# Kernel tuning notes

Measured on AMD Instinct MI355X. Metric: run time of the kernel, lower is better.

## Reference

```python
import jax, jax.numpy as jnp
import numpy as np

P, B, N, M, D_LAT = 4, 32, 2048, 512, 128
BETA = 1e-3
BIG = 1e9  # sentinel for masked-out pairwise distances


def quat_to_rotmat(q):
    # q: (..., 4) quaternion (w, x, y, z), normalized then converted
    q = q / jnp.linalg.norm(q, axis=-1, keepdims=True)
    w, x, y, z = q[..., 0], q[..., 1], q[..., 2], q[..., 3]
    R = jnp.stack([
        1 - 2 * (y * y + z * z), 2 * (x * y - w * z), 2 * (x * z + w * y),
        2 * (x * y + w * z), 1 - 2 * (x * x + z * z), 2 * (y * z - w * x),
        2 * (x * z - w * y), 2 * (y * z + w * x), 1 - 2 * (x * x + y * y),
    ], axis=-1)
    return R.reshape(q.shape[:-1] + (3, 3))


def setup_inputs() -> dict:
    key = jax.random.key(0)
    ks = jax.random.split(key, 8)
    return {
        'ipt': jax.random.normal(ks[0], (B, N, 3), jnp.float32),
        'opt': jax.random.normal(ks[1], (P, B, M, 3), jnp.float32),
        'trans': jax.random.normal(ks[2], (P, B, 3), jnp.float32),
        'rots': jax.random.normal(ks[3], (P, B, 4), jnp.float32),
        'probs': jax.random.uniform(ks[4], (P, B, 1), jnp.float32),
        'idx': jax.random.randint(ks[5], (B, N), 0, P),
        'mu': jax.random.normal(ks[6], (B, D_LAT), jnp.float32),
        'logvar': jax.random.normal(ks[7], (B, D_LAT), jnp.float32),
    }


def _parts_distance(ipt, opt, trans, rots, probs, idx):
    # Masked, fully-batched equivalent of the original python double loop:
    # index_select by (idx==i) + _remove_zero_rows are expressed as boolean
    # masks; empty part/sample combinations are excluded via `valid`.
    chamfer_d = 0.0
    coverage = 0.0
    quality = 0.0
    num = 0.0
    nonzero_x = jnp.any(ipt != 0, axis=-1)  # (B, N)
    for i in range(P):  # fixed small part count, structurally distinct slices
        y = opt[i]                                   # (B, M, 3)
        mask_y = jnp.any(y != 0, axis=-1)            # (B, M) _remove_zero_rows
        mx = (idx == i) & nonzero_x                  # (B, N) part selection
        # transform_to_primitives_centric_system: x_local = R (x - t)
        R = quat_to_rotmat(rots[i])                  # (B, 3, 3)
        x = jnp.einsum('bij,bnj->bni', R, ipt - trans[i][:, None, :])
        # pairwise squared distances, (B, N, M)
        D = jnp.sum((x[:, :, None, :] - y[:, None, :, :]) ** 2, axis=-1)
        nx = jnp.sum(mx, axis=-1)                    # (B,)
        ny = jnp.sum(mask_y, axis=-1)                # (B,)
        # quality: mean over valid x of min distance to valid y
        qual = jnp.sum(jnp.where(mx, jnp.min(jnp.where(mask_y[:, None, :], D, BIG), axis=-1), 0.0), axis=-1) / jnp.maximum(nx, 1)
        # coverage: mean over valid y of min distance to valid x
        cov = jnp.sum(jnp.where(mask_y, jnp.min(jnp.where(mx[:, :, None], D, BIG), axis=-2), 0.0), axis=-1) / jnp.maximum(ny, 1)
        cd = qual + cov                              # symmetric chamfer
        valid = (nx > 0) & (ny > 0)                  # x.size(0)!=0 and y.size(0)!=0
        w = jnp.where(valid, probs[i][:, 0], 0.0)    # prob-weighted sum over batch
        n = jnp.sum(valid).astype(jnp.float32)
        has = (n > 0).astype(jnp.float32)
        inv_n = has / jnp.maximum(n, 1.0)
        chamfer_d = chamfer_d + jnp.sum(w * cd) * inv_n
        coverage = coverage + jnp.sum(w * cov) * inv_n
        quality = quality + jnp.sum(w * qual) * inv_n
        num = num + has
    inv_num = 1.0 / jnp.maximum(num, 1.0)
    return chamfer_d * inv_num, coverage * inv_num, quality * inv_num


def KL(mu, logvar):
    # standard VAE KL: sum over latent, mean over batch
    return -0.5 * jnp.sum(1.0 + logvar - mu ** 2 - jnp.exp(logvar)) / mu.shape[0]


def reference(ipt, opt, trans, rots, probs, idx, mu, logvar):
    cds, covs, quals = _parts_distance(ipt, opt, trans, rots, probs, idx)
    kld = KL(mu, logvar)
    return (cds + BETA * kld, cds, covs, quals, kld)
```

## Files before the change

kernel.cpp:

```cpp
#include <hip/hip_runtime.h>
#include <math.h>

#define PP 4
#define BB 32
#define NN 2048
#define MM 512
#define DLAT 128
#define BETA_C 1e-3f
#define BIGV 1e9f
#define THREADS 512

__device__ float g_ws[4 * PP * BB];

__device__ __forceinline__ float dist2f4(float4 a, float4 b) {
    float dx = a.x - b.x, dy = a.y - b.y, dz = a.z - b.z;
    return dx * dx + dy * dy + dz * dz;
}

__global__ __launch_bounds__(THREADS) void parts_kernel(
    const float* __restrict__ ipt,
    const float* __restrict__ opt,
    const float* __restrict__ trans,
    const float* __restrict__ rots,
    const int*   __restrict__ idx)
{
    const int b = blockIdx.x;
    const int i = blockIdx.y;
    const int phase = blockIdx.z;
    const int tid = threadIdx.x;

    __shared__ float Rm[9], tv[3];
    __shared__ int s_nx, s_ny;
    __shared__ float4 sy[MM];
    __shared__ float4 sx[NN];
    __shared__ float red[THREADS / 64];

    if (tid == 0) {
        s_nx = 0;
        s_ny = 0;
        const float* q = rots + (i * BB + b) * 4;
        float qw = q[0], qx = q[1], qy = q[2], qz = q[3];
        float inv = 1.0f / sqrtf(qw * qw + qx * qx + qy * qy + qz * qz);
        qw *= inv; qx *= inv; qy *= inv; qz *= inv;
        Rm[0] = 1.0f - 2.0f * (qy * qy + qz * qz);
        Rm[1] = 2.0f * (qx * qy - qw * qz);
        Rm[2] = 2.0f * (qx * qz + qw * qy);
        Rm[3] = 2.0f * (qx * qy + qw * qz);
        Rm[4] = 1.0f - 2.0f * (qx * qx + qz * qz);
        Rm[5] = 2.0f * (qy * qz - qw * qx);
        Rm[6] = 2.0f * (qx * qz - qw * qy);
        Rm[7] = 2.0f * (qy * qz + qw * qx);
        Rm[8] = 1.0f - 2.0f * (qx * qx + qy * qy);
        const float* t = trans + (i * BB + b) * 3;
        tv[0] = t[0]; tv[1] = t[1]; tv[2] = t[2];
    }
    __syncthreads();

    int cnt = 0;
    for (int m = tid; m < MM; m += THREADS) {
        const float* y = opt + (((size_t)i * BB + b) * MM + m) * 3;
        float yx = y[0], yy = y[1], yz = y[2];
        bool v = (yx != 0.0f) | (yy != 0.0f) | (yz != 0.0f);
        if (v) cnt++;
        else { yx = 1e8f; yy = 1e8f; yz = 1e8f; }
        sy[m] = make_float4(yx, yy, yz, v ? 1.0f : 0.0f);
    }
    if (cnt) atomicAdd(&s_ny, cnt);

    const float R0 = Rm[0], R1 = Rm[1], R2 = Rm[2];
    const float R3 = Rm[3], R4 = Rm[4], R5 = Rm[5];
    const float R6 = Rm[6], R7 = Rm[7], R8 = Rm[8];
    const float t0 = tv[0], t1 = tv[1], t2 = tv[2];
    for (int n = tid; n < NN; n += THREADS) {
        const float* p = ipt + ((size_t)b * NN + n) * 3;
        float px = p[0], py = p[1], pz = p[2];
        bool nz = (px != 0.0f) | (py != 0.0f) | (pz != 0.0f);
        if (nz && idx[b * NN + n] == i) {
            px -= t0; py -= t1; pz -= t2;
            float lx = R0 * px + R1 * py + R2 * pz;
            float ly = R3 * px + R4 * py + R5 * pz;
            float lz = R6 * px + R7 * py + R8 * pz;
            int pos = atomicAdd(&s_nx, 1);
            sx[pos] = make_float4(lx, ly, lz, 0.0f);
        }
    }
    __syncthreads();
    const int nx = s_nx;
    const int ny = s_ny;

    float sum = 0.0f;
    if (phase == 0) {
        for (int k = tid; k < nx; k += THREADS) {
            float4 p = sx[k];
            float m0 = BIGV, m1 = BIGV, m2 = BIGV, m3 = BIGV;
            for (int m = 0; m < MM; m += 4) {
                m0 = fminf(m0, dist2f4(p, sy[m]));
                m1 = fminf(m1, dist2f4(p, sy[m + 1]));
                m2 = fminf(m2, dist2f4(p, sy[m + 2]));
                m3 = fminf(m3, dist2f4(p, sy[m + 3]));
            }
            sum += fminf(fminf(m0, m1), fminf(m2, m3));
        }
    } else {
        for (int m = tid; m < MM; m += THREADS) {
            float4 q = sy[m];
            if (q.w != 0.0f) {
                float m0 = BIGV, m1 = BIGV, m2 = BIGV, m3 = BIGV;
                int k = 0;
                for (; k + 4 <= nx; k += 4) {
                    m0 = fminf(m0, dist2f4(q, sx[k]));
                    m1 = fminf(m1, dist2f4(q, sx[k + 1]));
                    m2 = fminf(m2, dist2f4(q, sx[k + 2]));
                    m3 = fminf(m3, dist2f4(q, sx[k + 3]));
                }
                float dmin = fminf(fminf(m0, m1), fminf(m2, m3));
                for (; k < nx; ++k) dmin = fminf(dmin, dist2f4(q, sx[k]));
                sum += dmin;
            }
        }
    }

    for (int off = 32; off > 0; off >>= 1) sum += __shfl_down(sum, off);
    if ((tid & 63) == 0) red[tid >> 6] = sum;
    __syncthreads();
    if (tid == 0) {
        float tot = 0.0f;
        for (int w = 0; w < THREADS / 64; ++w) tot += red[w];
        int pb = i * BB + b;
        if (phase == 0) {
            g_ws[pb] = tot;
            g_ws[2 * PP * BB + pb] = (float)nx;
        } else {
            g_ws[PP * BB + pb] = tot;
            g_ws[3 * PP * BB + pb] = (float)ny;
        }
    }
}

__global__ __launch_bounds__(256) void finalize_kernel(
    const float* __restrict__ probs,
    const float* __restrict__ mu,
    const float* __restrict__ logvar,
    float* __restrict__ out)
{
    const int tid = threadIdx.x;
    __shared__ float red[4];
    __shared__ float s_wq[PP * BB], s_wc[PP * BB], s_val[PP * BB];

    float kls = 0.0f;
    for (int t = tid; t < BB * DLAT; t += 256) {
        float m_ = mu[t], lv = logvar[t];
        kls += 1.0f + lv - m_ * m_ - expf(lv);
    }
    for (int off = 32; off > 0; off >>= 1) kls += __shfl_down(kls, off);
    if ((tid & 63) == 0) red[tid >> 6] = kls;

    if (tid < PP * BB) {
        float qs = g_ws[tid];
        float cs = g_ws[PP * BB + tid];
        float nxf = g_ws[2 * PP * BB + tid];
        float nyf = g_ws[3 * PP * BB + tid];
        bool valid = (nxf > 0.0f) && (nyf > 0.0f);
        float w = valid ? probs[tid] : 0.0f;
        s_wq[tid] = w * (qs / fmaxf(nxf, 1.0f));
        s_wc[tid] = w * (cs / fmaxf(nyf, 1.0f));
        s_val[tid] = valid ? 1.0f : 0.0f;
    }
    __syncthreads();

    if (tid == 0) {
        float kld = -0.5f * (red[0] + red[1] + red[2] + red[3]) / (float)BB;
        float ch = 0.0f, cov = 0.0f, qu = 0.0f, num = 0.0f;
        for (int i = 0; i < PP; ++i) {
            float sq = 0.0f, sc = 0.0f, n = 0.0f;
            for (int bb = 0; bb < BB; ++bb) {
                sq += s_wq[i * BB + bb];
                sc += s_wc[i * BB + bb];
                n += s_val[i * BB + bb];
            }
            float has = (n > 0.0f) ? 1.0f : 0.0f;
            float invn = has / fmaxf(n, 1.0f);
            qu += sq * invn;
            cov += sc * invn;
            ch += (sq + sc) * invn;
            num += has;
        }
        float invnum = 1.0f / fmaxf(num, 1.0f);
        float cds = ch * invnum;
        out[0] = cds + BETA_C * kld;
        out[1] = cds;
        out[2] = cov * invnum;
        out[3] = qu * invnum;
        out[4] = kld;
    }
}

extern "C" void kernel_launch(void* const* d_in, const int* in_sizes, int n_in,
                              void* d_out, int out_size, void* d_ws, size_t ws_size,
                              hipStream_t stream) {
    const float* ipt    = (const float*)d_in[0];
    const float* opt    = (const float*)d_in[1];
    const float* trans  = (const float*)d_in[2];
    const float* rots   = (const float*)d_in[3];
    const float* probs  = (const float*)d_in[4];
    const int*   idx    = (const int*)d_in[5];
    const float* mu     = (const float*)d_in[6];
    const float* logvar = (const float*)d_in[7];
    float* out = (float*)d_out;
    (void)d_ws; (void)ws_size; (void)in_sizes; (void)n_in; (void)out_size;

    dim3 grid(BB, PP, 2);
    parts_kernel<<<grid, THREADS, 0, stream>>>(ipt, opt, trans, rots, idx);
    finalize_kernel<<<1, 256, 0, stream>>>(probs, mu, logvar, out);
}
```

Measured before the change: 108.6 us.

## Register-tile pairwise distance loops with SoA shared layout and 256-thread blocks

Switches the shared point buffers from float4 AoS to separate x/y/z arrays so each step loads four candidate coordinates with vector reads. Each thread now keeps several query points in registers and reuses every loaded target quad across them, raising arithmetic per shared-memory load. Block size drops to 256 threads, and the target array is padded with sentinels to a multiple of four so the tail loop goes away. In exchange it uses more registers per thread and gives fewer threads per block for the bandwidth-light setup phase.

```diff
diff --git a/kernel.cpp b/kernel.cpp
--- a/kernel.cpp
+++ b/kernel.cpp
@@ -8,13 +8,89 @@
 #define DLAT 128
 #define BETA_C 1e-3f
 #define BIGV 1e9f
-#define THREADS 512
+#define SENT 1e8f
+#define THREADS 256
 
 __device__ float g_ws[4 * PP * BB];
 
-__device__ __forceinline__ float dist2f4(float4 a, float4 b) {
-    float dx = a.x - b.x, dy = a.y - b.y, dz = a.z - b.z;
-    return dx * dx + dy * dy + dz * dz;
+template<int SLOTS>
+__device__ __forceinline__ float quality_pass(
+    const float* __restrict__ syx, const float* __restrict__ syy, const float* __restrict__ syz,
+    const float* __restrict__ sxx, const float* __restrict__ sxy, const float* __restrict__ sxz,
+    int nx, int base, int tid)
+{
+    float px[SLOTS], py[SLOTS], pz[SLOTS], mna[SLOTS], mnb[SLOTS];
+    bool act[SLOTS];
+#pragma unroll
+    for (int s = 0; s < SLOTS; ++s) {
+        int k = base + s * THREADS + tid;
+        act[s] = (k < nx);
+        px[s] = act[s] ? sxx[k] : SENT;
+        py[s] = act[s] ? sxy[k] : SENT;
+        pz[s] = act[s] ? sxz[k] : SENT;
+        mna[s] = BIGV; mnb[s] = BIGV;
+    }
+    for (int m = 0; m < MM; m += 4) {
+        float4 yx = *reinterpret_cast<const float4*>(syx + m);
+        float4 yy = *reinterpret_cast<const float4*>(syy + m);
+        float4 yz = *reinterpret_cast<const float4*>(syz + m);
+#pragma unroll
+        for (int s = 0; s < SLOTS; ++s) {
+            float dx0 = px[s] - yx.x, dy0 = py[s] - yy.x, dz0 = pz[s] - yz.x;
+            float dx1 = px[s] - yx.y, dy1 = py[s] - yy.y, dz1 = pz[s] - yz.y;
+            float dx2 = px[s] - yx.z, dy2 = py[s] - yy.z, dz2 = pz[s] - yz.z;
+            float dx3 = px[s] - yx.w, dy3 = py[s] - yy.w, dz3 = pz[s] - yz.w;
+            float d0 = dx0 * dx0 + dy0 * dy0 + dz0 * dz0;
+            float d1 = dx1 * dx1 + dy1 * dy1 + dz1 * dz1;
+            float d2 = dx2 * dx2 + dy2 * dy2 + dz2 * dz2;
+            float d3 = dx3 * dx3 + dy3 * dy3 + dz3 * dz3;
+            mna[s] = fminf(mna[s], fminf(d0, d1));
+            mnb[s] = fminf(mnb[s], fminf(d2, d3));
+        }
+    }
+    float sum = 0.0f;
+#pragma unroll
+    for (int s = 0; s < SLOTS; ++s)
+        if (act[s]) sum += fminf(mna[s], mnb[s]);
+    return sum;
+}
+
+__device__ __forceinline__ float coverage_pass(
+    const float* __restrict__ syx, const float* __restrict__ syy, const float* __restrict__ syz,
+    const float* __restrict__ sxx, const float* __restrict__ sxy, const float* __restrict__ sxz,
+    int nx4, int tid)
+{
+    float qx[2], qy[2], qz[2], mna[2], mnb[2];
+#pragma unroll
+    for (int s = 0; s < 2; ++s) {
+        int m = s * THREADS + tid;
+        qx[s] = syx[m]; qy[s] = syy[m]; qz[s] = syz[m];
+        mna[s] = BIGV; mnb[s] = BIGV;
+    }
+    for (int k = 0; k < nx4; k += 4) {
+        float4 xx = *reinterpret_cast<const float4*>(sxx + k);
+        float4 xy = *reinterpret_cast<const float4*>(sxy + k);
+        float4 xz = *reinterpret_cast<const float4*>(sxz + k);
+#pragma unroll
+        for (int s = 0; s < 2; ++s) {
+            float dx0 = qx[s] - xx.x, dy0 = qy[s] - xy.x, dz0 = qz[s] - xz.x;
+            float dx1 = qx[s] - xx.y, dy1 = qy[s] - xy.y, dz1 = qz[s] - xz.y;
+            float dx2 = qx[s] - xx.z, dy2 = qy[s] - xy.z, dz2 = qz[s] - xz.z;
+            float dx3 = qx[s] - xx.w, dy3 = qy[s] - xy.w, dz3 = qz[s] - xz.w;
+            float d0 = dx0 * dx0 + dy0 * dy0 + dz0 * dz0;
+            float d1 = dx1 * dx1 + dy1 * dy1 + dz1 * dz1;
+            float d2 = dx2 * dx2 + dy2 * dy2 + dz2 * dz2;
+            float d3 = dx3 * dx3 + dy3 * dy3 + dz3 * dz3;
+            mna[s] = fminf(mna[s], fminf(d0, d1));
+            mnb[s] = fminf(mnb[s], fminf(d2, d3));
+        }
+    }
+    float sum = 0.0f;
+#pragma unroll
+    for (int s = 0; s < 2; ++s)
+        if (qx[s] != SENT)
+            sum += fminf(mna[s], mnb[s]);
+    return sum;
 }
 
 __global__ __launch_bounds__(THREADS) void parts_kernel(
@@ -29,10 +105,10 @@
     const int phase = blockIdx.z;
     const int tid = threadIdx.x;
 
-    __shared__ float Rm[9], tv[3];
+    __shared__ float Rm[12];
     __shared__ int s_nx, s_ny;
-    __shared__ float4 sy[MM];
-    __shared__ float4 sx[NN];
+    __shared__ __align__(16) float syx[MM], syy[MM], syz[MM];
+    __shared__ __align__(16) float sxx[NN], sxy[NN], sxz[NN];
     __shared__ float red[THREADS / 64];
 
     if (tid == 0) {
@@ -52,7 +128,7 @@
         Rm[7] = 2.0f * (qy * qz + qw * qx);
         Rm[8] = 1.0f - 2.0f * (qx * qx + qy * qy);
         const float* t = trans + (i * BB + b) * 3;
-        tv[0] = t[0]; tv[1] = t[1]; tv[2] = t[2];
+        Rm[9] = t[0]; Rm[10] = t[1]; Rm[11] = t[2];
     }
     __syncthreads();
 
@@ -62,62 +138,47 @@
         float yx = y[0], yy = y[1], yz = y[2];
         bool v = (yx != 0.0f) | (yy != 0.0f) | (yz != 0.0f);
         if (v) cnt++;
-        else { yx = 1e8f; yy = 1e8f; yz = 1e8f; }
-        sy[m] = make_float4(yx, yy, yz, v ? 1.0f : 0.0f);
+        else { yx = SENT; yy = SENT; yz = SENT; }
+        syx[m] = yx; syy[m] = yy; syz[m] = yz;
     }
     if (cnt) atomicAdd(&s_ny, cnt);
 
     const float R0 = Rm[0], R1 = Rm[1], R2 = Rm[2];
     const float R3 = Rm[3], R4 = Rm[4], R5 = Rm[5];
     const float R6 = Rm[6], R7 = Rm[7], R8 = Rm[8];
-    const float t0 = tv[0], t1 = tv[1], t2 = tv[2];
+    const float t0 = Rm[9], t1 = Rm[10], t2 = Rm[11];
     for (int n = tid; n < NN; n += THREADS) {
         const float* p = ipt + ((size_t)b * NN + n) * 3;
         float px = p[0], py = p[1], pz = p[2];
         bool nz = (px != 0.0f) | (py != 0.0f) | (pz != 0.0f);
         if (nz && idx[b * NN + n] == i) {
             px -= t0; py -= t1; pz -= t2;
-            float lx = R0 * px + R1 * py + R2 * pz;
-            float ly = R3 * px + R4 * py + R5 * pz;
-            float lz = R6 * px + R7 * py + R8 * pz;
             int pos = atomicAdd(&s_nx, 1);
-            sx[pos] = make_float4(lx, ly, lz, 0.0f);
+            sxx[pos] = R0 * px + R1 * py + R2 * pz;
+            sxy[pos] = R3 * px + R4 * py + R5 * pz;
+            sxz[pos] = R6 * px + R7 * py + R8 * pz;
         }
     }
     __syncthreads();
     const int nx = s_nx;
     const int ny = s_ny;
-
-    float sum = 0.0f;
+    const int nx4 = (nx + 3) & ~3;
+    if (tid < nx4 - nx) {
+        sxx[nx + tid] = SENT; sxy[nx + tid] = SENT; sxz[nx + tid] = SENT;
+    }
+    __syncthreads();
+
+    float sum;
     if (phase == 0) {
-        for (int k = tid; k < nx; k += THREADS) {
-            float4 p = sx[k];
-            float m0 = BIGV, m1 = BIGV, m2 = BIGV, m3 = BIGV;
-            for (int m = 0; m < MM; m += 4) {
-                m0 = fminf(m0, dist2f4(p, sy[m]));
-                m1 = fminf(m1, dist2f4(p, sy[m + 1]));
-                m2 = fminf(m2, dist2f4(p, sy[m + 2]));
-                m3 = fminf(m3, dist2f4(p, sy[m + 3]));
-            }
-            sum += fminf(fminf(m0, m1), fminf(m2, m3));
+        if (nx <= 2 * THREADS) {
+            sum = quality_pass<2>(syx, syy, syz, sxx, sxy, sxz, nx, 0, tid);
+        } else {
+            sum = quality_pass<3>(syx, syy, syz, sxx, sxy, sxz, nx, 0, tid);
+            for (int k0 = 3 * THREADS; k0 < nx; k0 += THREADS)
+                sum += quality_pass<1>(syx, syy, syz, sxx, sxy, sxz, nx, k0, tid);
         }
     } else {
-        for (int m = tid; m < MM; m += THREADS) {
-            float4 q = sy[m];
-            if (q.w != 0.0f) {
-                float m0 = BIGV, m1 = BIGV, m2 = BIGV, m3 = BIGV;
-                int k = 0;
-                for (; k + 4 <= nx; k += 4) {
-                    m0 = fminf(m0, dist2f4(q, sx[k]));
-                    m1 = fminf(m1, dist2f4(q, sx[k + 1]));
-                    m2 = fminf(m2, dist2f4(q, sx[k + 2]));
-                    m3 = fminf(m3, dist2f4(q, sx[k + 3]));
-                }
-                float dmin = fminf(fminf(m0, m1), fminf(m2, m3));
-                for (; k < nx; ++k) dmin = fminf(dmin, dist2f4(q, sx[k]));
-                sum += dmin;
-            }
-        }
+        sum = coverage_pass(syx, syy, syz, sxx, sxy, sxz, nx4, tid);
     }
 
     for (int off = 32; off > 0; off >>= 1) sum += __shfl_down(sum, off);
```

Measured after the change: 110.2 us. Within noise of the previous version (+1.5%).
